# Optimization experiments

Hardware: AMD Instinct MI355X
Metric: run time of the kernel (lower is better)

Reference implementation:

```python
import jax, jax.numpy as jnp
import numpy as np

B, S, H, T = 64, 512, 768, 400


def setup_inputs() -> dict:
    key = jax.random.key(0)
    k1, k2 = jax.random.split(key)
    hidden = jax.random.normal(k1, (B, S, H), dtype=jnp.float32)
    # word_ids: non-decreasing piece->word map per sample, like HF tokenizer word_ids()
    word_ids = jnp.sort(jax.random.randint(k2, (B, S), 0, T), axis=-1).astype(jnp.int32)
    return {"hidden": hidden, "word_ids": word_ids, "num_tokens": T}


def reference(hidden, word_ids, num_tokens):
    # Ragged segment mean-pool: pool subword pieces into per-word reps.
    # hidden: [B, S, H] float; word_ids: [B, S] int in [0, num_tokens)
    b, s, h = hidden.shape
    # Flatten (sample, word) into one global segment id: sample*T + word
    seg = (jnp.arange(b, dtype=word_ids.dtype)[:, None] * num_tokens + word_ids).reshape(-1)
    sums = jax.ops.segment_sum(hidden.reshape(b * s, h), seg, num_segments=b * num_tokens)
    counts = jax.ops.segment_sum(jnp.ones((b * s,), hidden.dtype), seg, num_segments=b * num_tokens)
    # Words with zero pieces -> sum 0 / 1 = 0, matching torch.zeros fallback
    pooled = sums / jnp.maximum(counts, 1.0)[:, None]
    return pooled.reshape(b, num_tokens, h)
```

## Files before the change

### kernel.cpp

```cpp
#include <hip/hip_runtime.h>


#include <stdint.h>

#define BB 64
#define SS 512
#define HH 768
#define TT 400
#define LN (TT + 1)
#define NF4 (HH / 4)

__global__ __launch_bounds__(256) void bounds_kernel(
    const int* __restrict__ word_ids, int* __restrict__ L)
{
    const int b   = blockIdx.x;
    const int tid = threadIdx.x;

    __shared__ int s_w[SS];
    __shared__ int s_L[LN];

    const int2* r2 = reinterpret_cast<const int2*>(word_ids + b * SS);
    reinterpret_cast<int2*>(s_w)[tid] = r2[tid];
    for (int t = tid; t < LN; t += 256) s_L[t] = SS;
    __syncthreads();

    for (int s = tid; s < SS; s += 256) {
        const int w  = s_w[s];
        const int wp = (s == 0) ? -1 : s_w[s - 1];
        for (int t = wp + 1; t <= w; ++t) s_L[t] = s;
    }
    __syncthreads();

    int* Lb = L + b * LN;
    for (int t = tid; t < LN; t += 256) Lb[t] = s_L[t];
}

__global__ __launch_bounds__(256) void bert_lattice_pool_kernel(
    const float* __restrict__ hidden,
    const int* __restrict__ L,
    float* __restrict__ out)
{
    const int blk  = blockIdx.x;
    const int b    = blk / (TT / 4);
    const int q    = blk - b * (TT / 4);
    const int wv   = threadIdx.x >> 6;
    const int lane = threadIdx.x & 63;
    const int t    = q * 4 + wv;

    const int* Lb   = L + b * LN + t;
    const int start = Lb[0];
    const int end   = Lb[1];
    const int count = end - start;

    const float4* hp = reinterpret_cast<const float4*>(hidden)
                       + (size_t)(b * SS) * NF4;

    float4 a0 = make_float4(0.f, 0.f, 0.f, 0.f);
    float4 a1 = a0, a2 = a0;

    for (int s = start; s < end; ++s) {
        const float4* p = hp + (size_t)s * NF4;
        float4 v0 = p[lane];
        float4 v1 = p[lane + 64];
        float4 v2 = p[lane + 128];
        a0.x += v0.x; a0.y += v0.y; a0.z += v0.z; a0.w += v0.w;
        a1.x += v1.x; a1.y += v1.y; a1.z += v1.z; a1.w += v1.w;
        a2.x += v2.x; a2.y += v2.y; a2.z += v2.z; a2.w += v2.w;
    }

    const float inv = 1.0f / (float)(count > 0 ? count : 1);

    float4* o = reinterpret_cast<float4*>(out) + ((size_t)b * TT + t) * NF4;
    o[lane]       = make_float4(a0.x * inv, a0.y * inv, a0.z * inv, a0.w * inv);
    o[lane + 64]  = make_float4(a1.x * inv, a1.y * inv, a1.z * inv, a1.w * inv);
    o[lane + 128] = make_float4(a2.x * inv, a2.y * inv, a2.z * inv, a2.w * inv);
}

extern "C" void kernel_launch(void* const* d_in, const int* in_sizes, int n_in,
                              void* d_out, int out_size, void* d_ws, size_t ws_size,
                              hipStream_t stream) {
    (void)in_sizes; (void)n_in; (void)ws_size; (void)out_size;
    const float* hidden   = (const float*)d_in[0];
    const int*   word_ids = (const int*)d_in[1];
    float*       out      = (float*)d_out;
    int*         L        = (int*)d_ws;

    bounds_kernel<<<dim3(BB), dim3(256), 0, stream>>>(word_ids, L);

    bert_lattice_pool_kernel<<<dim3(BB * TT / 4), dim3(256), 0, stream>>>(
        hidden, L, out);
}
```

Before: 176.1 us.

## Pool two words per wave in a grid-stride loop with nontemporal accesses

Each wave now handles two adjacent words, walking their combined piece range in one loop and sending each row to one of two accumulator sets. The grid is fixed at 1600 blocks and loops over jobs. Loads and stores use nontemporal builtins so the streamed data bypasses cache retention. The goal is to cut per-word launch and scheduling overhead and to improve streaming bandwidth, at the cost of fewer waves in flight and a per-row branch.

Measured after the change: 174.2 us. Within noise of the previous version (-1.1%).

```diff
diff --git a/kernel.cpp b/kernel.cpp
--- a/kernel.cpp
+++ b/kernel.cpp
@@ -1,7 +1,6 @@
 #include <hip/hip_runtime.h>
+#include <stdint.h>
 
-
-#include <stdint.h>
 
 #define BB 64
 #define SS 512
@@ -9,6 +8,11 @@
 #define TT 400
 #define LN (TT + 1)
 #define NF4 (HH / 4)
+#define JPB (TT / 8)
+#define NJ  (BB * JPB)
+#define GRID 1600
+
+typedef float f4 __attribute__((ext_vector_type(4)));
 
 __global__ __launch_bounds__(256) void bounds_kernel(
     const int* __restrict__ word_ids, int* __restrict__ L)
@@ -40,40 +44,52 @@
     const int* __restrict__ L,
     float* __restrict__ out)
 {
-    const int blk  = blockIdx.x;
-    const int b    = blk / (TT / 4);
-    const int q    = blk - b * (TT / 4);
     const int wv   = threadIdx.x >> 6;
     const int lane = threadIdx.x & 63;
-    const int t    = q * 4 + wv;
+    const f4 z4 = {0.f, 0.f, 0.f, 0.f};
 
-    const int* Lb   = L + b * LN + t;
-    const int start = Lb[0];
-    const int end   = Lb[1];
-    const int count = end - start;
+    for (int job = blockIdx.x; job < NJ; job += GRID) {
+        const int b  = job / JPB;
+        const int t0 = (job - b * JPB) * 8 + wv * 2;
 
-    const float4* hp = reinterpret_cast<const float4*>(hidden)
+        const int* Lb = L + b * LN + t0;
+        const int s0 = Lb[0];
+        const int e0 = Lb[1];
+        const int e1 = Lb[2];
+
+        const f4* hp = reinterpret_cast<const f4*>(hidden)
                        + (size_t)(b * SS) * NF4;
 
-    float4 a0 = make_float4(0.f, 0.f, 0.f, 0.f);
-    float4 a1 = a0, a2 = a0;
+        f4 p0 = z4, p1 = z4, p2 = z4;
+        f4 q0 = z4, q1 = z4, q2 = z4;
 
-    for (int s = start; s < end; ++s) {
-        const float4* p = hp + (size_t)s * NF4;
-        float4 v0 = p[lane];
-        float4 v1 = p[lane + 64];
-        float4 v2 = p[lane + 128];
-        a0.x += v0.x; a0.y += v0.y; a0.z += v0.z; a0.w += v0.w;
-        a1.x += v1.x; a1.y += v1.y; a1.z += v1.z; a1.w += v1.w;
-        a2.x += v2.x; a2.y += v2.y; a2.z += v2.z; a2.w += v2.w;
+        for (int s = s0; s < e1; ++s) {
+            const f4* p = hp + (size_t)s * NF4;
+            const f4 v0 = __builtin_nontemporal_load(p + lane);
+            const f4 v1 = __builtin_nontemporal_load(p + lane + 64);
+            const f4 v2 = __builtin_nontemporal_load(p + lane + 128);
+            if (s < e0) {
+                p0 += v0; p1 += v1; p2 += v2;
+            } else {
+                q0 += v0; q1 += v1; q2 += v2;
+            }
+        }
+
+        const int   c0 = e0 - s0;
+        const int   c1 = e1 - e0;
+        const float i0 = 1.0f / (float)(c0 > 0 ? c0 : 1);
+        const float i1 = 1.0f / (float)(c1 > 0 ? c1 : 1);
+
+        f4* o0 = reinterpret_cast<f4*>(out) + ((size_t)b * TT + t0) * NF4;
+        f4* o1 = o0 + NF4;
+
+        __builtin_nontemporal_store(p0 * i0, o0 + lane);
+        __builtin_nontemporal_store(p1 * i0, o0 + lane + 64);
+        __builtin_nontemporal_store(p2 * i0, o0 + lane + 128);
+        __builtin_nontemporal_store(q0 * i1, o1 + lane);
+        __builtin_nontemporal_store(q1 * i1, o1 + lane + 64);
+        __builtin_nontemporal_store(q2 * i1, o1 + lane + 128);
     }
-
-    const float inv = 1.0f / (float)(count > 0 ? count : 1);
-
-    float4* o = reinterpret_cast<float4*>(out) + ((size_t)b * TT + t) * NF4;
-    o[lane]       = make_float4(a0.x * inv, a0.y * inv, a0.z * inv, a0.w * inv);
-    o[lane + 64]  = make_float4(a1.x * inv, a1.y * inv, a1.z * inv, a1.w * inv);
-    o[lane + 128] = make_float4(a2.x * inv, a2.y * inv, a2.z * inv, a2.w * inv);
 }
 
 extern "C" void kernel_launch(void* const* d_in, const int* in_sizes, int n_in,
@@ -86,7 +102,6 @@
     int*         L        = (int*)d_ws;
 
     bounds_kernel<<<dim3(BB), dim3(256), 0, stream>>>(word_ids, L);
-
-    bert_lattice_pool_kernel<<<dim3(BB * TT / 4), dim3(256), 0, stream>>>(
+    bert_lattice_pool_kernel<<<dim3(GRID), dim3(256), 0, stream>>>(
         hidden, L, out);
 }
```

## Process four words per wavefront with unrolled loads, XCD swizzle, nontemporal access

Applied to the files above, without the earlier changes.

Each wavefront now pools four consecutive words over their contiguous piece range, so the block grid shrinks and per-word load latency is amortised by loading two rows per iteration. Block indices are remapped so consecutive logical chunks land on the same XCD, and loads and stores use nontemporal hints to avoid polluting cache with streamed data. In exchange it uses more accumulator registers, adds per-row branching to pick the target word, and reduces the number of blocks, which may hurt latency hiding.

Result: faster. 170.7 us (-3.1%).

```diff
diff --git a/kernel.cpp b/kernel.cpp
--- a/kernel.cpp
+++ b/kernel.cpp
@@ -1,7 +1,6 @@
 #include <hip/hip_runtime.h>
+#include <stdint.h>
 
-
-#include <stdint.h>
 
 #define BB 64
 #define SS 512
@@ -9,6 +8,14 @@
 #define TT 400
 #define LN (TT + 1)
 #define NF4 (HH / 4)
+#define WPW 4
+#define WPB 16
+#define CPS (TT / WPB)
+#define NBLK (BB * CPS)
+#define NXCD 8
+#define BPX (NBLK / NXCD)
+
+typedef float f4 __attribute__((ext_vector_type(4)));
 
 __global__ __launch_bounds__(256) void bounds_kernel(
     const int* __restrict__ word_ids, int* __restrict__ L)
@@ -40,40 +47,86 @@
     const int* __restrict__ L,
     float* __restrict__ out)
 {
-    const int blk  = blockIdx.x;
-    const int b    = blk / (TT / 4);
-    const int q    = blk - b * (TT / 4);
-    const int wv   = threadIdx.x >> 6;
+    const int p  = blockIdx.x;
+    const int q  = (p % NXCD) * BPX + p / NXCD;
+    const int b  = q / CPS;
+    const int w0 = (q - b * CPS) * WPB + (threadIdx.x >> 6) * WPW;
     const int lane = threadIdx.x & 63;
-    const int t    = q * 4 + wv;
 
-    const int* Lb   = L + b * LN + t;
-    const int start = Lb[0];
-    const int end   = Lb[1];
-    const int count = end - start;
+    const int* Lb = L + b * LN + w0;
+    const int b0 = Lb[0], b1 = Lb[1], b2 = Lb[2], b3 = Lb[3], b4 = Lb[4];
 
-    const float4* hp = reinterpret_cast<const float4*>(hidden)
-                       + (size_t)(b * SS) * NF4;
+    const f4* hp = reinterpret_cast<const f4*>(hidden)
+                   + (size_t)(b * SS) * NF4 + lane;
 
-    float4 a0 = make_float4(0.f, 0.f, 0.f, 0.f);
-    float4 a1 = a0, a2 = a0;
+    const f4 z4 = {0.f, 0.f, 0.f, 0.f};
+    f4 a00 = z4, a01 = z4, a02 = z4;
+    f4 a10 = z4, a11 = z4, a12 = z4;
+    f4 a20 = z4, a21 = z4, a22 = z4;
+    f4 a30 = z4, a31 = z4, a32 = z4;
 
-    for (int s = start; s < end; ++s) {
-        const float4* p = hp + (size_t)s * NF4;
-        float4 v0 = p[lane];
-        float4 v1 = p[lane + 64];
-        float4 v2 = p[lane + 128];
-        a0.x += v0.x; a0.y += v0.y; a0.z += v0.z; a0.w += v0.w;
-        a1.x += v1.x; a1.y += v1.y; a1.z += v1.z; a1.w += v1.w;
-        a2.x += v2.x; a2.y += v2.y; a2.z += v2.z; a2.w += v2.w;
+    int s = b0;
+    const int send = b4;
+    const int smax = send - 1;
+    int t = 0;
+    int e = b1;
+
+#define ADD_ROW(V0, V1, V2, SR)                                        \
+    do {                                                               \
+        while ((SR) >= e) { ++t; e = (t == 1) ? b2 : (t == 2) ? b3 : b4; } \
+        switch (t) {                                                   \
+            case 0: a00 += (V0); a01 += (V1); a02 += (V2); break;      \
+            case 1: a10 += (V0); a11 += (V1); a12 += (V2); break;      \
+            case 2: a20 += (V0); a21 += (V1); a22 += (V2); break;      \
+            default: a30 += (V0); a31 += (V1); a32 += (V2); break;     \
+        }                                                              \
+    } while (0)
+
+    while (s < send) {
+        const int s1c = (s + 1 > smax) ? smax : s + 1;
+        const f4* p0 = hp + (size_t)s * NF4;
+        const f4* p1 = hp + (size_t)s1c * NF4;
+        const f4 u0 = __builtin_nontemporal_load(p0);
+        const f4 u1 = __builtin_nontemporal_load(p0 + 64);
+        const f4 u2 = __builtin_nontemporal_load(p0 + 128);
+        const f4 v0 = __builtin_nontemporal_load(p1);
+        const f4 v1 = __builtin_nontemporal_load(p1 + 64);
+        const f4 v2 = __builtin_nontemporal_load(p1 + 128);
+
+        ADD_ROW(u0, u1, u2, s);
+        if (s + 1 < send) ADD_ROW(v0, v1, v2, s + 1);
+        s += 2;
     }
+#undef ADD_ROW
 
-    const float inv = 1.0f / (float)(count > 0 ? count : 1);
-
-    float4* o = reinterpret_cast<float4*>(out) + ((size_t)b * TT + t) * NF4;
-    o[lane]       = make_float4(a0.x * inv, a0.y * inv, a0.z * inv, a0.w * inv);
-    o[lane + 64]  = make_float4(a1.x * inv, a1.y * inv, a1.z * inv, a1.w * inv);
-    o[lane + 128] = make_float4(a2.x * inv, a2.y * inv, a2.z * inv, a2.w * inv);
+    f4* o = reinterpret_cast<f4*>(out) + ((size_t)b * TT + w0) * NF4 + lane;
+    {
+        const int c = b1 - b0; const float inv = 1.0f / (float)(c > 0 ? c : 1);
+        __builtin_nontemporal_store(a00 * inv, o);
+        __builtin_nontemporal_store(a01 * inv, o + 64);
+        __builtin_nontemporal_store(a02 * inv, o + 128);
+    }
+    o += NF4;
+    {
+        const int c = b2 - b1; const float inv = 1.0f / (float)(c > 0 ? c : 1);
+        __builtin_nontemporal_store(a10 * inv, o);
+        __builtin_nontemporal_store(a11 * inv, o + 64);
+        __builtin_nontemporal_store(a12 * inv, o + 128);
+    }
+    o += NF4;
+    {
+        const int c = b3 - b2; const float inv = 1.0f / (float)(c > 0 ? c : 1);
+        __builtin_nontemporal_store(a20 * inv, o);
+        __builtin_nontemporal_store(a21 * inv, o + 64);
+        __builtin_nontemporal_store(a22 * inv, o + 128);
+    }
+    o += NF4;
+    {
+        const int c = b4 - b3; const float inv = 1.0f / (float)(c > 0 ? c : 1);
+        __builtin_nontemporal_store(a30 * inv, o);
+        __builtin_nontemporal_store(a31 * inv, o + 64);
+        __builtin_nontemporal_store(a32 * inv, o + 128);
+    }
 }
 
 extern "C" void kernel_launch(void* const* d_in, const int* in_sizes, int n_in,
@@ -86,7 +139,6 @@
     int*         L        = (int*)d_ws;
 
     bounds_kernel<<<dim3(BB), dim3(256), 0, stream>>>(word_ids, L);
-
-    bert_lattice_pool_kernel<<<dim3(BB * TT / 4), dim3(256), 0, stream>>>(
+    bert_lattice_pool_kernel<<<dim3(NBLK), dim3(256), 0, stream>>>(
         hidden, L, out);
 }
```

## Balance segment-pool work by row chunks per wave with XCD-aware block mapping

Applied to the files above, without the earlier changes.

Instead of one wave per word, each sample's 512 rows are split into 64 equal chunks, and each wave handles the words whose pieces start in its chunk. The chunk-to-word boundaries are found by binary search in the bounds kernel. The main loop is unrolled by two rows, uses nontemporal loads and stores, and reads word boundaries through lane shuffles. Blocks are remapped so neighbouring samples land on the same XCD. The aim is to balance load across waves and cut the per-word launch and latency overhead, at the cost of more complex control flow with divergent close and zero-fill branches.

After: 174.8 us. No clear change (-0.8%).

```diff
diff --git a/kernel.cpp b/kernel.cpp
--- a/kernel.cpp
+++ b/kernel.cpp
@@ -1,7 +1,6 @@
 #include <hip/hip_runtime.h>
+#include <stdint.h>
 
-
-#include <stdint.h>
 
 #define BB 64
 #define SS 512
@@ -9,9 +8,18 @@
 #define TT 400
 #define LN (TT + 1)
 #define NF4 (HH / 4)
+#define NWS 64
+#define RPW (SS / NWS)
+#define BPS (NWS / 4)
+#define NBLK (BB * BPS)
+#define NXCD 8
+#define BPX (NBLK / NXCD)
+#define PN  (NWS + 1)
+
+typedef float f4 __attribute__((ext_vector_type(4)));
 
 __global__ __launch_bounds__(256) void bounds_kernel(
-    const int* __restrict__ word_ids, int* __restrict__ L)
+    const int* __restrict__ word_ids, int* __restrict__ L, int* __restrict__ P)
 {
     const int b   = blockIdx.x;
     const int tid = threadIdx.x;
@@ -33,47 +41,102 @@
 
     int* Lb = L + b * LN;
     for (int t = tid; t < LN; t += 256) Lb[t] = s_L[t];
+
+    if (tid < NWS) {
+        const int target = tid * RPW;
+        int lo = 0, hi = TT;
+        while (lo < hi) {
+            const int m = (lo + hi) >> 1;
+            if (s_L[m] < target) lo = m + 1; else hi = m;
+        }
+        P[b * PN + tid] = lo;
+    }
+    if (tid == NWS) P[b * PN + NWS] = TT;
 }
 
 __global__ __launch_bounds__(256) void bert_lattice_pool_kernel(
     const float* __restrict__ hidden,
     const int* __restrict__ L,
+    const int* __restrict__ P,
     float* __restrict__ out)
 {
-    const int blk  = blockIdx.x;
-    const int b    = blk / (TT / 4);
-    const int q    = blk - b * (TT / 4);
-    const int wv   = threadIdx.x >> 6;
+    const int p    = blockIdx.x;
+    const int q    = (p % NXCD) * BPX + p / NXCD;
+    const int b    = q / BPS;
+    const int kin  = (q - b * BPS) * 4 + (threadIdx.x >> 6);
     const int lane = threadIdx.x & 63;
-    const int t    = q * 4 + wv;
 
-    const int* Lb   = L + b * LN + t;
-    const int start = Lb[0];
-    const int end   = Lb[1];
-    const int count = end - start;
+    const int* Lb = L + b * LN;
+    const int* Pb = P + b * PN;
+    const int P0 = Pb[kin];
+    const int P1 = Pb[kin + 1];
+    if (P0 >= P1) return;
 
-    const float4* hp = reinterpret_cast<const float4*>(hidden)
-                       + (size_t)(b * SS) * NF4;
+    const int Lidx = (P0 + lane <= TT) ? P0 + lane : TT;
+    const int Lreg = Lb[Lidx];
 
-    float4 a0 = make_float4(0.f, 0.f, 0.f, 0.f);
-    float4 a1 = a0, a2 = a0;
+#define GETL(i)  ({ const int i_ = (i) <= TT ? (i) : TT;                   \
+                    const int d_ = i_ - P0;                                \
+                    (d_ < 64) ? __shfl(Lreg, d_) : Lb[i_]; })
 
-    for (int s = start; s < end; ++s) {
-        const float4* p = hp + (size_t)s * NF4;
-        float4 v0 = p[lane];
-        float4 v1 = p[lane + 64];
-        float4 v2 = p[lane + 128];
-        a0.x += v0.x; a0.y += v0.y; a0.z += v0.z; a0.w += v0.w;
-        a1.x += v1.x; a1.y += v1.y; a1.z += v1.z; a1.w += v1.w;
-        a2.x += v2.x; a2.y += v2.y; a2.z += v2.z; a2.w += v2.w;
+    const int rbeg = GETL(P0);
+    const int rend = GETL(P1);
+
+    float* outp = out + (size_t)b * TT * HH;
+    const f4 z4 = {0.f, 0.f, 0.f, 0.f};
+
+#define ZWORD(tt) do {                                                     \
+        f4* o_ = reinterpret_cast<f4*>(outp + (size_t)(tt) * HH) + lane;   \
+        __builtin_nontemporal_store(z4, o_);                               \
+        __builtin_nontemporal_store(z4, o_ + 64);                          \
+        __builtin_nontemporal_store(z4, o_ + 128);                         \
+    } while (0)
+
+    int t  = P0;
+    int ws = rbeg;
+    int e  = GETL(P0 + 1);
+
+    while (t < P1 && e == ws) { ZWORD(t); ++t; ws = e; e = GETL(t + 1); }
+
+    f4 a0 = z4, a1 = z4, a2 = z4;
+
+#define CLOSE() do {                                                       \
+        const float inv = 1.0f / (float)(e - ws);                          \
+        f4* o_ = reinterpret_cast<f4*>(outp + (size_t)t * HH) + lane;      \
+        __builtin_nontemporal_store(a0 * inv, o_);                         \
+        __builtin_nontemporal_store(a1 * inv, o_ + 64);                    \
+        __builtin_nontemporal_store(a2 * inv, o_ + 128);                   \
+        a0 = z4; a1 = z4; a2 = z4;                                         \
+        ++t; ws = e; e = GETL(t + 1);                                      \
+        while (t < P1 && e == ws) { ZWORD(t); ++t; ws = e; e = GETL(t + 1); } \
+    } while (0)
+
+    const f4* hp = reinterpret_cast<const f4*>(hidden)
+                   + (size_t)(b * SS) * NF4 + lane;
+
+    int s = rbeg;
+    while (s < rend) {
+        const int s1c = (s + 1 < SS) ? s + 1 : SS - 1;
+        const f4* p0 = hp + (size_t)s   * NF4;
+        const f4* p1 = hp + (size_t)s1c * NF4;
+        const f4 u0 = __builtin_nontemporal_load(p0);
+        const f4 u1 = __builtin_nontemporal_load(p0 + 64);
+        const f4 u2 = __builtin_nontemporal_load(p0 + 128);
+        const f4 v0 = __builtin_nontemporal_load(p1);
+        const f4 v1 = __builtin_nontemporal_load(p1 + 64);
+        const f4 v2 = __builtin_nontemporal_load(p1 + 128);
+
+        a0 += u0; a1 += u1; a2 += u2;
+        if (s + 1 == e) CLOSE();
+        if (s + 1 < rend) {
+            a0 += v0; a1 += v1; a2 += v2;
+            if (s + 2 == e) CLOSE();
+        }
+        s += 2;
     }
-
-    const float inv = 1.0f / (float)(count > 0 ? count : 1);
-
-    float4* o = reinterpret_cast<float4*>(out) + ((size_t)b * TT + t) * NF4;
-    o[lane]       = make_float4(a0.x * inv, a0.y * inv, a0.z * inv, a0.w * inv);
-    o[lane + 64]  = make_float4(a1.x * inv, a1.y * inv, a1.z * inv, a1.w * inv);
-    o[lane + 128] = make_float4(a2.x * inv, a2.y * inv, a2.z * inv, a2.w * inv);
+#undef CLOSE
+#undef ZWORD
+#undef GETL
 }
 
 extern "C" void kernel_launch(void* const* d_in, const int* in_sizes, int n_in,
@@ -84,9 +147,9 @@
     const int*   word_ids = (const int*)d_in[1];
     float*       out      = (float*)d_out;
     int*         L        = (int*)d_ws;
+    int*         P        = L + BB * LN;
 
-    bounds_kernel<<<dim3(BB), dim3(256), 0, stream>>>(word_ids, L);
-
-    bert_lattice_pool_kernel<<<dim3(BB * TT / 4), dim3(256), 0, stream>>>(
-        hidden, L, out);
+    bounds_kernel<<<dim3(BB), dim3(256), 0, stream>>>(word_ids, L, P);
+    bert_lattice_pool_kernel<<<dim3(NBLK), dim3(256), 0, stream>>>(
+        hidden, L, P, out);
 }
```
